# Performance work log

Hardware: AMD Instinct MI355X
Metric: run time of the kernel (lower is better)

## Reference

```python
import jax, jax.numpy as jnp
import numpy as np

B, CIN, COUT, COFF, H, W = 4, 256, 256, 256, 64, 64
DG, K = 16, 3            # deformable groups, kernel size
KK = K * K               # 9 taps


def _conv3x3(x, w, b):
    y = jax.lax.conv_general_dilated(x, w, window_strides=(1, 1), padding='SAME',
                                     dimension_numbers=('NCHW', 'OIHW', 'NCHW'))
    return y + b[None, :, None, None]


def _bilinear_sample(xg, ys, xs):
    # xg: [B,DG,Cg,H,W]; ys,xs: [B,DG,Ho,Wo] float sampling coords (zero padding outside)
    Bn, dg, Cg, Hh, Ww = xg.shape
    xf = xg.reshape(Bn, dg, Cg, Hh * Ww)
    y0 = jnp.floor(ys)
    x0 = jnp.floor(xs)
    wy = (ys - y0)[:, :, None]  # [B,DG,1,Ho,Wo]
    wx = (xs - x0)[:, :, None]

    def gather(yi, xi):
        valid = (yi >= 0) & (yi < Hh) & (xi >= 0) & (xi < Ww)
        yc = jnp.clip(yi, 0, Hh - 1).astype(jnp.int32)
        xc = jnp.clip(xi, 0, Ww - 1).astype(jnp.int32)
        idx = (yc * Ww + xc).reshape(Bn, dg, 1, -1)
        v = jnp.take_along_axis(xf, jnp.broadcast_to(idx, (Bn, dg, Cg, idx.shape[-1])), axis=-1)
        v = v.reshape(Bn, dg, Cg, ys.shape[2], ys.shape[3])
        return v * valid[:, :, None].astype(xg.dtype)

    v00 = gather(y0, x0)
    v01 = gather(y0, x0 + 1)
    v10 = gather(y0 + 1, x0)
    v11 = gather(y0 + 1, x0 + 1)
    return v00 * (1 - wy) * (1 - wx) + v01 * (1 - wy) * wx + v10 * wy * (1 - wx) + v11 * wy * wx


def _deform_conv2d(x, offset, mask, weight, bias):
    # torchvision modulated deform_conv2d, stride=1, padding=1, dilation=1, groups=1
    Bn, C, Hh, Ww = x.shape
    Cg = C // DG
    xg = x.reshape(Bn, DG, Cg, Hh, Ww)
    # offset channel layout: 2*(g*KK + k) -> dy, +1 -> dx
    off = offset.reshape(Bn, DG, KK, 2, Hh, Ww)
    msk = mask.reshape(Bn, DG, KK, Hh, Ww)
    wk = weight.reshape(weight.shape[0], DG, Cg, K, K)
    hb = jnp.arange(Hh, dtype=x.dtype)[:, None]
    wb = jnp.arange(Ww, dtype=x.dtype)[None, :]
    acc = jnp.zeros((Bn, weight.shape[0], Hh, Ww), dtype=x.dtype)
    for ki in range(K):
        for kj in range(K):
            k = ki * K + kj
            ys = hb - 1 + ki + off[:, :, k, 0]   # padding=1, dilation=1
            xs = wb - 1 + kj + off[:, :, k, 1]
            s = _bilinear_sample(xg, ys, xs) * msk[:, :, k][:, :, None]  # [B,DG,Cg,H,W]
            acc = acc + jnp.einsum('bgchw,ogc->bohw', s, wk[:, :, :, ki, kj])
    return acc + bias[None, :, None, None]


def setup_inputs() -> dict:
    key = jax.random.key(0)
    ks = jax.random.split(key, 10)
    s = 0.02
    return {
        'x': jax.random.normal(ks[0], (B, CIN, H, W), jnp.float32),
        'offset_feat': jax.random.normal(ks[1], (B, COFF, H, W), jnp.float32),
        'weight': jax.random.normal(ks[2], (COUT, CIN, K, K), jnp.float32) * s,
        'bias': jax.random.normal(ks[3], (COUT,), jnp.float32) * s,
        'w1': jax.random.normal(ks[4], (COUT, COFF, K, K), jnp.float32) * s,
        'b1': jax.random.normal(ks[5], (COUT,), jnp.float32) * s,
        'w2': jax.random.normal(ks[6], (COUT, COUT, K, K), jnp.float32) * s,
        'b2': jax.random.normal(ks[7], (COUT,), jnp.float32) * s,
        'w3': jax.random.normal(ks[8], (27 * DG, COUT, K, K), jnp.float32) * 0.01,
        'b3': jax.random.normal(ks[9], (27 * DG,), jnp.float32) * 0.01,
    }


def reference(x, offset_feat, weight, bias, w1, b1, w2, b2, w3, b3):
    out = jax.nn.silu(_conv3x3(offset_feat, w1, b1))
    out = jax.nn.silu(_conv3x3(out, w2, b2))
    out = _conv3x3(out, w3, b3)                 # [B, 27*DG, H, W]
    o1, o2, m = jnp.split(out, 3, axis=1)
    offset = jnp.concatenate([o1, o2], axis=1)  # [B, 2*DG*9, H, W]
    mask = jax.nn.sigmoid(m)                    # [B, DG*9, H, W]
    return _deform_conv2d(x, offset, mask, weight, bias)
```

## Files before the change

### kernel.cpp

```cpp
#include <hip/hip_runtime.h>
#include <math.h>

typedef __attribute__((ext_vector_type(8))) short  bf16x8;
typedef __attribute__((ext_vector_type(8))) unsigned short u16x8;
typedef __attribute__((ext_vector_type(4))) float  f32x4;

__device__ __forceinline__ float b2f(unsigned short h) {
  return __uint_as_float(((unsigned int)h) << 16);
}
__device__ __forceinline__ unsigned short f2bf(float f) {
  unsigned int u = __float_as_uint(f);
  unsigned int r = (u + 0x7fffu + ((u >> 16) & 1u)) >> 16;
  return (unsigned short)r;
}
__device__ __forceinline__ void gload16(const unsigned short* g, unsigned short* l) {
  __builtin_amdgcn_global_load_lds(
      (const __attribute__((address_space(1))) void*)g,
      (__attribute__((address_space(3))) void*)l, 16, 0, 0);
}

__global__ __launch_bounds__(256) void nhwc_kernel(const float* __restrict__ in,
                                                   unsigned short* __restrict__ out) {
  const int y = blockIdx.x, b = blockIdx.y;
  const int t = threadIdx.x;
  __shared__ float lds[64 * 65];
  for (int c0 = 0; c0 < 256; c0 += 64) {
    #pragma unroll
    for (int i = 0; i < 16; ++i) {
      int cl = i * 4 + (t >> 6);
      int xx = t & 63;
      lds[cl * 65 + xx] = in[(((size_t)b * 256 + c0 + cl) * 64 + y) * 64 + xx];
    }
    __syncthreads();
    #pragma unroll
    for (int i = 0; i < 16; ++i) {
      int xx = i * 4 + (t >> 6);
      int cl = t & 63;
      out[(((size_t)b * 64 + y) * 64 + xx) * 256 + c0 + cl] = f2bf(lds[cl * 65 + xx]);
    }
    __syncthreads();
  }
}

__global__ __launch_bounds__(256) void wprep_kernel(const float* __restrict__ w,
                                                    unsigned short* __restrict__ Wp,
                                                    int COUT_valid) {
  const int kk = blockIdx.x;
  const int co = blockIdx.y;
  const int ci = threadIdx.x;
  float v = (co < COUT_valid) ? w[((size_t)co * 256 + ci) * 9 + kk] : 0.0f;
  Wp[(size_t)co * 2304 + kk * 256 + ci] = f2bf(v);
}

__global__ __launch_bounds__(256) void sampler_kernel(const float* __restrict__ t3,
                                                      const unsigned short* __restrict__ xh,
                                                      unsigned short* __restrict__ S) {
  const int t = threadIdx.x;
  const int g = t & 15;
  const int m = blockIdx.x * 16 + (t >> 4);
  const int b = m >> 12, pix = m & 4095, y = pix >> 6, x = pix & 63;
  const float* off = t3 + (size_t)m * 432;

  #pragma unroll
  for (int kk = 0; kk < 9; ++kk) {
    const int ki = kk / 3, kj = kk % 3;
    float dyv = off[2 * (g * 9 + kk)];
    float dxv = off[2 * (g * 9 + kk) + 1];
    float ml  = off[288 + g * 9 + kk];
    float mk  = 1.0f / (1.0f + __expf(-ml));
    float ysf = (float)(y - 1 + ki) + dyv;
    float xsf = (float)(x - 1 + kj) + dxv;
    float y0f = floorf(ysf), x0f = floorf(xsf);
    float wy = ysf - y0f, wx = xsf - x0f;
    int yi0 = (int)y0f, xi0 = (int)x0f;
    int yi1 = yi0 + 1, xi1 = xi0 + 1;
    bool vy0 = (yi0 >= 0) && (yi0 < 64), vy1 = (yi1 >= 0) && (yi1 < 64);
    bool vx0 = (xi0 >= 0) && (xi0 < 64), vx1 = (xi1 >= 0) && (xi1 < 64);
    int yc0 = min(max(yi0, 0), 63), yc1 = min(max(yi1, 0), 63);
    int xc0 = min(max(xi0, 0), 63), xc1 = min(max(xi1, 0), 63);
    float w00 = (vy0 && vx0) ? (1.f - wy) * (1.f - wx) * mk : 0.f;
    float w01 = (vy0 && vx1) ? (1.f - wy) * wx * mk : 0.f;
    float w10 = (vy1 && vx0) ? wy * (1.f - wx) * mk : 0.f;
    float w11 = (vy1 && vx1) ? wy * wx * mk : 0.f;

    float sacc[16];
    #pragma unroll
    for (int c = 0; c < 16; ++c) sacc[c] = 0.f;

    const size_t bbase = (size_t)(b << 12) * 256 + g * 16;
    const int p00 = yc0 * 64 + xc0, p01 = yc0 * 64 + xc1;
    const int p10 = yc1 * 64 + xc0, p11 = yc1 * 64 + xc1;
    {
      u16x8 lo = *(const u16x8*)(xh + bbase + (size_t)p00 * 256);
      u16x8 hi = *(const u16x8*)(xh + bbase + (size_t)p00 * 256 + 8);
      #pragma unroll
      for (int j = 0; j < 8; ++j) { sacc[j] += w00 * b2f(lo[j]); sacc[8 + j] += w00 * b2f(hi[j]); }
    }
    {
      u16x8 lo = *(const u16x8*)(xh + bbase + (size_t)p01 * 256);
      u16x8 hi = *(const u16x8*)(xh + bbase + (size_t)p01 * 256 + 8);
      #pragma unroll
      for (int j = 0; j < 8; ++j) { sacc[j] += w01 * b2f(lo[j]); sacc[8 + j] += w01 * b2f(hi[j]); }
    }
    {
      u16x8 lo = *(const u16x8*)(xh + bbase + (size_t)p10 * 256);
      u16x8 hi = *(const u16x8*)(xh + bbase + (size_t)p10 * 256 + 8);
      #pragma unroll
      for (int j = 0; j < 8; ++j) { sacc[j] += w10 * b2f(lo[j]); sacc[8 + j] += w10 * b2f(hi[j]); }
    }
    {
      u16x8 lo = *(const u16x8*)(xh + bbase + (size_t)p11 * 256);
      u16x8 hi = *(const u16x8*)(xh + bbase + (size_t)p11 * 256 + 8);
      #pragma unroll
      for (int j = 0; j < 8; ++j) { sacc[j] += w11 * b2f(lo[j]); sacc[8 + j] += w11 * b2f(hi[j]); }
    }
    u16x8 olo, ohi;
    #pragma unroll
    for (int j = 0; j < 8; ++j) { olo[j] = f2bf(sacc[j]); ohi[j] = f2bf(sacc[8 + j]); }
    unsigned short* sp = S + (size_t)m * 2304 + kk * 256 + g * 16;
    *(u16x8*)sp = olo;
    *(u16x8*)(sp + 8) = ohi;
  }
}

template<int EPI, bool IMPLICIT>
__global__ __launch_bounds__(256, 2) void gemm_kernel(
    const unsigned short* __restrict__ A,
    const unsigned short* __restrict__ W,
    const float* __restrict__ bias,
    void* __restrict__ outp,
    const unsigned short* __restrict__ zbuf,
    int K, int Nvalid) {
  constexpr int BM = 128, BN = 64, BK = 64;
  constexpr int NSTEP = 36;
  __shared__ unsigned short lds[2][(BM + BN) * BK];

  const int t = threadIdx.x, lane = t & 63, w = t >> 6;
  const int wm = w >> 1, wn = w & 1;
  const int m0 = blockIdx.x * BM, n0 = blockIdx.y * BN;

  const unsigned short* baseA[4];
  const unsigned short* zsrcA[4];
  unsigned int vmaskA[4];
  #pragma unroll
  for (int i = 0; i < 4; ++i) {
    int c   = (i * 4 + w) * 64 + lane;
    int row = c >> 3;
    int ccl = (c & 7) ^ (row & 7);
    int m   = m0 + row;
    if (IMPLICIT) {
      int y = (m >> 6) & 63, x = m & 63;
      unsigned int vm = 0;
      #pragma unroll
      for (int kk = 0; kk < 9; ++kk) {
        int dy = kk / 3 - 1, dx = kk % 3 - 1;
        if ((unsigned)(y + dy) < 64u && (unsigned)(x + dx) < 64u) vm |= (1u << kk);
      }
      vmaskA[i] = vm;
      baseA[i] = A + (size_t)m * 256 + ccl * 8;
      zsrcA[i] = zbuf + ccl * 8;
    } else {
      baseA[i] = A + (size_t)m * K + ccl * 8;
      zsrcA[i] = zbuf;
      vmaskA[i] = 0;
    }
  }
  const unsigned short* baseB[2];
  #pragma unroll
  for (int j = 0; j < 2; ++j) {
    int c   = (16 + j * 4 + w) * 64 + lane;
    int row = (c - 1024) >> 3;
    int ccl = (c & 7) ^ (row & 7);
    baseB[j] = W + (size_t)(n0 + row) * K + ccl * 8;
  }

  int offA[4][2], offB[2][2];
  #pragma unroll
  for (int mi = 0; mi < 4; ++mi) {
    int r = wm * 64 + mi * 16 + (lane & 15);
    #pragma unroll
    for (int kh = 0; kh < 2; ++kh) {
      int ccl = kh * 4 + (lane >> 4);
      offA[mi][kh] = r * 64 + ((ccl ^ (r & 7)) * 8);
    }
  }
  #pragma unroll
  for (int nj = 0; nj < 2; ++nj) {
    int r = wn * 32 + nj * 16 + (lane & 15);
    #pragma unroll
    for (int kh = 0; kh < 2; ++kh) {
      int ccl = kh * 4 + (lane >> 4);
      offB[nj][kh] = BM * BK + r * 64 + ((ccl ^ (r & 7)) * 8);
    }
  }

  f32x4 acc[4][2];
  #pragma unroll
  for (int mi = 0; mi < 4; ++mi)
    #pragma unroll
    for (int nj = 0; nj < 2; ++nj) acc[mi][nj] = (f32x4){0.f, 0.f, 0.f, 0.f};

  auto STAGE = [&](int sn, unsigned short* buf) {
    if (IMPLICIT) {
      int kkn = sn >> 2;
      int ci0 = (sn & 3) * 64;
      int q3  = kkn / 3;
      int soff = ((q3 - 1) * 64 + (kkn - q3 * 3 - 1)) * 256 + ci0;
      #pragma unroll
      for (int i = 0; i < 4; ++i) {
        const unsigned short* src = ((vmaskA[i] >> kkn) & 1u) ? baseA[i] + soff : zsrcA[i];
        gload16(src, buf + (i * 4 + w) * 512);
      }
    } else {
      #pragma unroll
      for (int i = 0; i < 4; ++i)
        gload16(baseA[i] + (size_t)sn * 64, buf + (i * 4 + w) * 512);
    }
    #pragma unroll
    for (int j = 0; j < 2; ++j)
      gload16(baseB[j] + (size_t)sn * 64, buf + 8192 + (j * 4 + w) * 512);
  };

  STAGE(0, lds[0]);

  for (int s = 0; s < NSTEP; ++s) {
    unsigned short* cur = lds[s & 1];
    if (s + 1 < NSTEP) {
      STAGE(s + 1, lds[(s + 1) & 1]);
      asm volatile("s_waitcnt vmcnt(6)" ::: "memory");
    } else {
      asm volatile("s_waitcnt vmcnt(0)" ::: "memory");
    }
    __builtin_amdgcn_s_barrier();
    __builtin_amdgcn_sched_barrier(0);

    bf16x8 af[4][2], bfg[2][2];
    #pragma unroll
    for (int mi = 0; mi < 4; ++mi)
      #pragma unroll
      for (int kh = 0; kh < 2; ++kh)
        af[mi][kh] = *(const bf16x8*)&cur[offA[mi][kh]];
    #pragma unroll
    for (int nj = 0; nj < 2; ++nj)
      #pragma unroll
      for (int kh = 0; kh < 2; ++kh)
        bfg[nj][kh] = *(const bf16x8*)&cur[offB[nj][kh]];

    #pragma unroll
    for (int kh = 0; kh < 2; ++kh)
      #pragma unroll
      for (int mi = 0; mi < 4; ++mi)
        #pragma unroll
        for (int nj = 0; nj < 2; ++nj)
          acc[mi][nj] = __builtin_amdgcn_mfma_f32_16x16x32_bf16(af[mi][kh], bfg[nj][kh],
                                                                acc[mi][nj], 0, 0, 0);
    __builtin_amdgcn_sched_barrier(0);
    asm volatile("s_waitcnt lgkmcnt(0)" ::: "memory");
    __builtin_amdgcn_s_barrier();
  }

  const int gmBase = m0 + wm * 64 + (lane >> 4) * 4;
  const int gnBase = n0 + wn * 32 + (lane & 15);
  #pragma unroll
  for (int nj = 0; nj < 2; ++nj) {
    const int gn = gnBase + nj * 16;
    const float bv = (gn < Nvalid) ? bias[gn] : 0.f;
    #pragma unroll
    for (int mi = 0; mi < 4; ++mi) {
      #pragma unroll
      for (int r = 0; r < 4; ++r) {
        const int gm = gmBase + mi * 16 + r;
        float v = acc[mi][nj][r] + bv;
        if (EPI == 0) {
          float sv = v / (1.0f + __expf(-v));
          ((unsigned short*)outp)[(size_t)gm * 256 + gn] = f2bf(sv);
        } else if (EPI == 1) {
          if (gn < Nvalid) ((float*)outp)[(size_t)gm * 432 + gn] = v;
        } else {
          ((float*)outp)[((size_t)(gm >> 12) * 256 + gn) * 4096 + (gm & 4095)] = v;
        }
      }
    }
  }
}

extern "C" void kernel_launch(void* const* d_in, const int* in_sizes, int n_in,
                              void* d_out, int out_size, void* d_ws, size_t ws_size,
                              hipStream_t stream) {
  const float* x      = (const float*)d_in[0];
  const float* offeat = (const float*)d_in[1];
  const float* weight = (const float*)d_in[2];
  const float* bias   = (const float*)d_in[3];
  const float* w1     = (const float*)d_in[4];
  const float* b1     = (const float*)d_in[5];
  const float* w2     = (const float*)d_in[6];
  const float* b2     = (const float*)d_in[7];
  const float* w3     = (const float*)d_in[8];
  const float* b3     = (const float*)d_in[9];
  float* out = (float*)d_out;

  char* ws = (char*)d_ws;
  unsigned short* xh  = (unsigned short*)(ws + 0);
  float*          t3  = (float*)(ws + 8388608);
  unsigned short* Wd  = (unsigned short*)(ws + 36700160);
  unsigned short* zb  = (unsigned short*)(ws + 37879808);
  unsigned short* S   = (unsigned short*)(ws + 37880064);
  unsigned short* fh  = (unsigned short*)(ws + 37880064);
  unsigned short* t1  = (unsigned short*)(ws + 46268672);
  unsigned short* t2  = (unsigned short*)(ws + 54657280);
  unsigned short* W1p = (unsigned short*)(ws + 63045888);
  unsigned short* W2p = (unsigned short*)(ws + 64225536);
  unsigned short* W3p = (unsigned short*)(ws + 65405184);

  hipMemsetAsync(zb, 0, 256, stream);

  nhwc_kernel<<<dim3(64, 4), 256, 0, stream>>>(x, xh);
  nhwc_kernel<<<dim3(64, 4), 256, 0, stream>>>(offeat, fh);
  wprep_kernel<<<dim3(9, 256), 256, 0, stream>>>(w1, W1p, 256);
  wprep_kernel<<<dim3(9, 256), 256, 0, stream>>>(w2, W2p, 256);
  wprep_kernel<<<dim3(9, 448), 256, 0, stream>>>(w3, W3p, 432);
  wprep_kernel<<<dim3(9, 256), 256, 0, stream>>>(weight, Wd, 256);

  gemm_kernel<0, true><<<dim3(128, 4), 256, 0, stream>>>(fh, W1p, b1, t1, zb, 2304, 256);
  gemm_kernel<0, true><<<dim3(128, 4), 256, 0, stream>>>(t1, W2p, b2, t2, zb, 2304, 256);
  gemm_kernel<1, true><<<dim3(128, 7), 256, 0, stream>>>(t2, W3p, b3, t3, zb, 2304, 432);

  sampler_kernel<<<dim3(1024), 256, 0, stream>>>(t3, xh, S);
  gemm_kernel<2, false><<<dim3(128, 4), 256, 0, stream>>>(S, Wd, bias, out, zb, 2304, 256);
}
```

Baseline: 209.3 us.

## Load GEMM A tiles directly to registers, stage weights via padded LDS

The GEMM kernel now reads A fragments straight from global memory into registers instead of staging them through LDS with async global-to-LDS loads. Only the weight (B) tile goes through a double-buffered, padded LDS layout, prefetched into registers one step ahead. Blocks are also remapped across the eight XCDs so neighbouring M tiles share an L2. This drops LDS traffic and frees LDS, but A loads are no longer prefetched ahead of the MFMAs, so their global latency may be exposed, and A is fetched once per warp column rather than shared within the block.

```diff
diff --git a/kernel.cpp b/kernel.cpp
--- a/kernel.cpp
+++ b/kernel.cpp
@@ -12,11 +12,6 @@
   unsigned int u = __float_as_uint(f);
   unsigned int r = (u + 0x7fffu + ((u >> 16) & 1u)) >> 16;
   return (unsigned short)r;
-}
-__device__ __forceinline__ void gload16(const unsigned short* g, unsigned short* l) {
-  __builtin_amdgcn_global_load_lds(
-      (const __attribute__((address_space(1))) void*)g,
-      (__attribute__((address_space(3))) void*)l, 16, 0, 0);
 }
 
 __global__ __launch_bounds__(256) void nhwc_kernel(const float* __restrict__ in,
@@ -123,31 +118,35 @@
   }
 }
 
-template<int EPI, bool IMPLICIT>
+template<int EPI, bool IMPLICIT, int NB>
 __global__ __launch_bounds__(256, 2) void gemm_kernel(
     const unsigned short* __restrict__ A,
-    const unsigned short* __restrict__ W,
+    const unsigned short* __restrict__ Wb,
     const float* __restrict__ bias,
     void* __restrict__ outp,
     const unsigned short* __restrict__ zbuf,
     int K, int Nvalid) {
-  constexpr int BM = 128, BN = 64, BK = 64;
+  constexpr int BM = 128;
   constexpr int NSTEP = 36;
-  __shared__ unsigned short lds[2][(BM + BN) * BK];
+  constexpr int LDSW = 72;
+  __shared__ unsigned short ldsB0[64 * LDSW];
+  __shared__ unsigned short ldsB1[64 * LDSW];
 
   const int t = threadIdx.x, lane = t & 63, w = t >> 6;
   const int wm = w >> 1, wn = w & 1;
-  const int m0 = blockIdx.x * BM, n0 = blockIdx.y * BN;
+
+  const int bid = blockIdx.x;
+  const int xcd = bid & 7, slot = bid >> 3;
+  const int by = slot % NB, bxl = slot / NB;
+  const int m0 = (bxl * 8 + xcd) * BM;
+  const int n0 = by * 64;
 
   const unsigned short* baseA[4];
-  const unsigned short* zsrcA[4];
   unsigned int vmaskA[4];
-  #pragma unroll
-  for (int i = 0; i < 4; ++i) {
-    int c   = (i * 4 + w) * 64 + lane;
-    int row = c >> 3;
-    int ccl = (c & 7) ^ (row & 7);
-    int m   = m0 + row;
+  const unsigned short* zsrc = zbuf + (lane >> 4) * 8;
+  #pragma unroll
+  for (int mi = 0; mi < 4; ++mi) {
+    int m = m0 + wm * 64 + mi * 16 + (lane & 15);
     if (IMPLICIT) {
       int y = (m >> 6) & 63, x = m & 63;
       unsigned int vm = 0;
@@ -156,42 +155,27 @@
         int dy = kk / 3 - 1, dx = kk % 3 - 1;
         if ((unsigned)(y + dy) < 64u && (unsigned)(x + dx) < 64u) vm |= (1u << kk);
       }
-      vmaskA[i] = vm;
-      baseA[i] = A + (size_t)m * 256 + ccl * 8;
-      zsrcA[i] = zbuf + ccl * 8;
+      vmaskA[mi] = vm;
+      baseA[mi] = A + (size_t)m * 256 + (lane >> 4) * 8;
     } else {
-      baseA[i] = A + (size_t)m * K + ccl * 8;
-      zsrcA[i] = zbuf;
-      vmaskA[i] = 0;
-    }
-  }
-  const unsigned short* baseB[2];
-  #pragma unroll
-  for (int j = 0; j < 2; ++j) {
-    int c   = (16 + j * 4 + w) * 64 + lane;
-    int row = (c - 1024) >> 3;
-    int ccl = (c & 7) ^ (row & 7);
-    baseB[j] = W + (size_t)(n0 + row) * K + ccl * 8;
-  }
-
-  int offA[4][2], offB[2][2];
-  #pragma unroll
-  for (int mi = 0; mi < 4; ++mi) {
-    int r = wm * 64 + mi * 16 + (lane & 15);
-    #pragma unroll
-    for (int kh = 0; kh < 2; ++kh) {
-      int ccl = kh * 4 + (lane >> 4);
-      offA[mi][kh] = r * 64 + ((ccl ^ (r & 7)) * 8);
-    }
-  }
+      vmaskA[mi] = 0;
+      baseA[mi] = A + (size_t)m * K + (lane >> 4) * 8;
+    }
+  }
+
+  const int snr = t >> 3, skc = t & 7;
+  const unsigned short* srcB0 = Wb + (size_t)(n0 + snr) * K + skc * 8;
+  const unsigned short* srcB1 = Wb + (size_t)(n0 + 32 + snr) * K + skc * 8;
+  const int woff0 = snr * LDSW + skc * 8;
+  const int woff1 = woff0 + 32 * LDSW;
+
+  int offB[2][2];
   #pragma unroll
   for (int nj = 0; nj < 2; ++nj) {
-    int r = wn * 32 + nj * 16 + (lane & 15);
-    #pragma unroll
-    for (int kh = 0; kh < 2; ++kh) {
-      int ccl = kh * 4 + (lane >> 4);
-      offB[nj][kh] = BM * BK + r * 64 + ((ccl ^ (r & 7)) * 8);
-    }
+    int n = wn * 32 + nj * 16 + (lane & 15);
+    #pragma unroll
+    for (int kh = 0; kh < 2; ++kh)
+      offB[nj][kh] = n * LDSW + (kh * 4 + (lane >> 4)) * 8;
   }
 
   f32x4 acc[4][2];
@@ -200,51 +184,48 @@
     #pragma unroll
     for (int nj = 0; nj < 2; ++nj) acc[mi][nj] = (f32x4){0.f, 0.f, 0.f, 0.f};
 
-  auto STAGE = [&](int sn, unsigned short* buf) {
+  {
+    bf16x8 b0 = *(const bf16x8*)srcB0;
+    bf16x8 b1 = *(const bf16x8*)srcB1;
+    *(bf16x8*)&ldsB0[woff0] = b0;
+    *(bf16x8*)&ldsB1[0] = b1;
+    *(bf16x8*)&ldsB0[woff1] = b1;
+    asm volatile("s_waitcnt lgkmcnt(0)" ::: "memory");
+    __builtin_amdgcn_s_barrier();
+  }
+
+  auto STEP = [&](int s, const unsigned short* rb, unsigned short* wb) {
+    const bool stage = (s + 1 < NSTEP);
+    bf16x8 breg0, breg1;
+    if (stage) {
+      breg0 = *(const bf16x8*)(srcB0 + (size_t)(s + 1) * 64);
+      breg1 = *(const bf16x8*)(srcB1 + (size_t)(s + 1) * 64);
+    }
+    bf16x8 af[4][2];
     if (IMPLICIT) {
-      int kkn = sn >> 2;
-      int ci0 = (sn & 3) * 64;
-      int q3  = kkn / 3;
-      int soff = ((q3 - 1) * 64 + (kkn - q3 * 3 - 1)) * 256 + ci0;
-      #pragma unroll
-      for (int i = 0; i < 4; ++i) {
-        const unsigned short* src = ((vmaskA[i] >> kkn) & 1u) ? baseA[i] + soff : zsrcA[i];
-        gload16(src, buf + (i * 4 + w) * 512);
+      int kkn = s >> 2;
+      int q3 = kkn / 3;
+      int soff = ((q3 - 1) * 64 + (kkn - q3 * 3 - 1)) * 256 + (s & 3) * 64;
+      #pragma unroll
+      for (int mi = 0; mi < 4; ++mi) {
+        const unsigned short* p = ((vmaskA[mi] >> kkn) & 1u) ? baseA[mi] + soff : zsrc;
+        af[mi][0] = *(const bf16x8*)p;
+        af[mi][1] = *(const bf16x8*)(p + 32);
       }
     } else {
       #pragma unroll
-      for (int i = 0; i < 4; ++i)
-        gload16(baseA[i] + (size_t)sn * 64, buf + (i * 4 + w) * 512);
-    }
-    #pragma unroll
-    for (int j = 0; j < 2; ++j)
-      gload16(baseB[j] + (size_t)sn * 64, buf + 8192 + (j * 4 + w) * 512);
-  };
-
-  STAGE(0, lds[0]);
-
-  for (int s = 0; s < NSTEP; ++s) {
-    unsigned short* cur = lds[s & 1];
-    if (s + 1 < NSTEP) {
-      STAGE(s + 1, lds[(s + 1) & 1]);
-      asm volatile("s_waitcnt vmcnt(6)" ::: "memory");
-    } else {
-      asm volatile("s_waitcnt vmcnt(0)" ::: "memory");
-    }
-    __builtin_amdgcn_s_barrier();
-    __builtin_amdgcn_sched_barrier(0);
-
-    bf16x8 af[4][2], bfg[2][2];
-    #pragma unroll
-    for (int mi = 0; mi < 4; ++mi)
+      for (int mi = 0; mi < 4; ++mi) {
+        const unsigned short* p = baseA[mi] + s * 64;
+        af[mi][0] = *(const bf16x8*)p;
+        af[mi][1] = *(const bf16x8*)(p + 32);
+      }
+    }
+    bf16x8 bfg[2][2];
+    #pragma unroll
+    for (int nj = 0; nj < 2; ++nj)
       #pragma unroll
       for (int kh = 0; kh < 2; ++kh)
-        af[mi][kh] = *(const bf16x8*)&cur[offA[mi][kh]];
-    #pragma unroll
-    for (int nj = 0; nj < 2; ++nj)
-      #pragma unroll
-      for (int kh = 0; kh < 2; ++kh)
-        bfg[nj][kh] = *(const bf16x8*)&cur[offB[nj][kh]];
+        bfg[nj][kh] = *(const bf16x8*)&rb[offB[nj][kh]];
 
     #pragma unroll
     for (int kh = 0; kh < 2; ++kh)
@@ -254,9 +235,18 @@
         for (int nj = 0; nj < 2; ++nj)
           acc[mi][nj] = __builtin_amdgcn_mfma_f32_16x16x32_bf16(af[mi][kh], bfg[nj][kh],
                                                                 acc[mi][nj], 0, 0, 0);
-    __builtin_amdgcn_sched_barrier(0);
-    asm volatile("s_waitcnt lgkmcnt(0)" ::: "memory");
-    __builtin_amdgcn_s_barrier();
+    if (stage) {
+      *(bf16x8*)&wb[woff0] = breg0;
+      *(bf16x8*)&wb[woff1] = breg1;
+      asm volatile("s_waitcnt lgkmcnt(0)" ::: "memory");
+      __builtin_amdgcn_s_barrier();
+    }
+  };
+
+  #pragma unroll 1
+  for (int ss = 0; ss < NSTEP; ss += 2) {
+    STEP(ss,     ldsB0, ldsB1);
+    STEP(ss + 1, ldsB1, ldsB0);
   }
 
   const int gmBase = m0 + wm * 64 + (lane >> 4) * 4;
@@ -321,10 +311,10 @@
   wprep_kernel<<<dim3(9, 448), 256, 0, stream>>>(w3, W3p, 432);
   wprep_kernel<<<dim3(9, 256), 256, 0, stream>>>(weight, Wd, 256);
 
-  gemm_kernel<0, true><<<dim3(128, 4), 256, 0, stream>>>(fh, W1p, b1, t1, zb, 2304, 256);
-  gemm_kernel<0, true><<<dim3(128, 4), 256, 0, stream>>>(t1, W2p, b2, t2, zb, 2304, 256);
-  gemm_kernel<1, true><<<dim3(128, 7), 256, 0, stream>>>(t2, W3p, b3, t3, zb, 2304, 432);
+  gemm_kernel<0, true, 4><<<dim3(512), 256, 0, stream>>>(fh, W1p, b1, t1, zb, 2304, 256);
+  gemm_kernel<0, true, 4><<<dim3(512), 256, 0, stream>>>(t1, W2p, b2, t2, zb, 2304, 256);
+  gemm_kernel<1, true, 7><<<dim3(896), 256, 0, stream>>>(t2, W3p, b3, t3, zb, 2304, 432);
 
   sampler_kernel<<<dim3(1024), 256, 0, stream>>>(t3, xh, S);
-  gemm_kernel<2, false><<<dim3(128, 4), 256, 0, stream>>>(S, Wd, bias, out, zb, 2304, 256);
-}
+  gemm_kernel<2, false, 4><<<dim3(512), 256, 0, stream>>>(S, Wd, bias, out, zb, 2304, 256);
+}
```

Result: slower. 465.9 us (+122.6%).
